# Optimization experiments

Measured on AMD Instinct MI355X. Metric: run time of the kernel, lower is better.

## Reference

```python
import jax, jax.numpy as jnp
import numpy as np
import math

PERIODS = [4, 2, 1]          # period_num[-3:] sorted desc
SEQ, PRED, CH = 192, 96, 8
TOPM, DM = 20, 512
N_TRAIN, BSZ = 10000, 32


def decompose_mg(data):
    # data: [N, L, C] -> mg: [P, N, L, C], offset-removed (last step per period)
    N, L, C = data.shape
    mgs = []
    for g in PERIODS:
        cur = data.reshape(N, L // g, g, C).mean(axis=2)   # pooled
        cur = jnp.repeat(cur, g, axis=1)                   # repeat_interleave
        mgs.append(cur)
    mg = jnp.stack(mgs, axis=0)                            # [P, N, L, C]
    offset = mg[:, :, -1:, :]
    return mg - offset


def l2norm(x, eps=1e-12):
    n = jnp.sqrt(jnp.sum(x * x, axis=-1, keepdims=True))
    return x / jnp.maximum(n, eps)


def setup_inputs() -> dict:
    key = jax.random.key(0)
    ks = jax.random.split(key, 10)
    F = SEQ * CH
    return {
        "x": jax.random.normal(ks[0], (BSZ, SEQ, CH), dtype=jnp.float32),
        "index": jax.random.randint(ks[1], (BSZ,), 0, N_TRAIN),
        "train_data_all": jax.random.normal(ks[2], (N_TRAIN, SEQ, CH), dtype=jnp.float32),
        "y_data_all": jax.random.normal(ks[3], (N_TRAIN, PRED, CH), dtype=jnp.float32),
        "W_sim": jax.random.normal(ks[4], (F, F), dtype=jnp.float32) / math.sqrt(F),
        "b_sim": jax.random.normal(ks[5], (F,), dtype=jnp.float32) * 0.01,
        "Wq": jax.random.normal(ks[6], (CH, DM), dtype=jnp.float32) / math.sqrt(CH),
        "bq": jax.random.normal(ks[7], (DM,), dtype=jnp.float32) * 0.01,
        "Wk": jax.random.normal(ks[8], (CH, DM), dtype=jnp.float32) / math.sqrt(CH),
        "bk": jax.random.normal(ks[9], (DM,), dtype=jnp.float32) * 0.01,
    }


def reference(x, index, train_data_all, y_data_all, W_sim, b_sim, Wq, bq, Wk, bk):
    P = len(PERIODS)
    bsz = x.shape[0]
    n_train = train_data_all.shape[0]

    # multi-period decomposition (prepare_dataset + retrieve)
    train_mg = decompose_mg(train_data_all)   # [P, N, SEQ, CH]
    y_mg = decompose_mg(y_data_all)           # [P, N, PRED, CH]
    x_mg = decompose_mg(x)                    # [P, B, SEQ, CH]

    # periodic_batch_corr: shared linear then cosine similarity
    bx = x_mg.reshape(P, bsz, -1) @ W_sim + b_sim           # [P, B, F]
    ax = train_mg.reshape(P, n_train, -1) @ W_sim + b_sim   # [P, N, F]
    sim = jnp.einsum('pbf,pnf->pbn', l2norm(bx), l2norm(ax))

    # self-exclusion sliding mask (train=True)
    win = 2 * (SEQ + PRED) - 1
    slid = jnp.arange(win)[None, :] + (index - SEQ - PRED + 1)[:, None]
    slid = jnp.clip(slid, 0, n_train - 1)
    mask = jnp.zeros((bsz, n_train), dtype=bool).at[
        jnp.arange(bsz)[:, None], slid].set(True)
    sim = jnp.where(mask[None], -jnp.inf, sim)

    # top-m retrieval
    _, topm_idx = jax.lax.top_k(sim, TOPM)                  # [P, B, TOPM]

    # gather neighbors per period
    gather = jax.vmap(lambda src, i: src[i])                # over period axis
    k = gather(train_mg, topm_idx)                          # [P, B, M, SEQ, CH]
    v = gather(y_mg, topm_idx)                              # [P, B, M, PRED, CH]

    # cross attention (shared projections across periods)
    q_emb = x_mg @ Wq + bq                                  # [P, B, S, D]
    k_emb = k @ Wk + bk                                     # [P, B, M, T, D]
    scores = jnp.einsum('pbsd,pbmtd->pbsmt', q_emb, k_emb) / math.sqrt(DM)
    S = scores.shape[2]
    w = jax.nn.softmax(scores.reshape(P, bsz, S, TOPM * S), axis=-1)
    w = w.reshape(P, bsz, S, TOPM, S)
    nw = w.sum(axis=-1).sum(axis=2)                         # [P, B, M]
    nw = jax.nn.softmax(nw, axis=-1)
    out = jnp.einsum('pbm,pbmlc->pblc', nw, v)              # [P, B, PRED, CH]
    return out
```

## Files before the change

### kernel.cpp

```cpp
#include <hip/hip_runtime.h>
#include <hip/hip_bf16.h>
#include <math.h>

#define NPER 3
#define SEQL 192
#define PREDL 96
#define CH 8
#define FD 1536
#define NT 10000
#define BS 32
#define PB 96
#define TOPM 20
#define DM 512
#define HALFW 287
#define NROWS 30000
#define NRP2 10112
#define NRB2 79
#define NCB 12
#define PCOLS 24
#define NWG2 (NRB2*NCB)
#define NJ 3840
#define K0R 384
#define K1R 768
#define K2R 1536
#define KS 16
#define NCH 4
#define CHSZ (NT/NCH)
#define NWTG 4080
#define NB_DOT (3*NRB2)
#define RSQRT_DM 0.04419417382415922f

typedef __attribute__((ext_vector_type(8))) short bf16x8;
typedef __attribute__((ext_vector_type(4))) float f32x4;
typedef __attribute__((address_space(3))) short lds_short_t;
typedef __attribute__((address_space(1))) const short glb_short_t;

__device__ inline float bflo(unsigned u){ return __uint_as_float(u << 16); }
__device__ inline float bfhi(unsigned u){ return __uint_as_float(u & 0xFFFF0000u); }
__device__ inline float bf2f(unsigned short u){ return __uint_as_float((unsigned)u << 16); }
__device__ inline unsigned short f2bf(float v){
  __hip_bfloat16 h = __float2bfloat16(v);
  return *reinterpret_cast<unsigned short*>(&h);
}

template<int L>
__device__ __forceinline__ void dec_body(const float* __restrict__ data,
                                         float* __restrict__ mg,
                                         __hip_bfloat16* __restrict__ m0,
                                         __hip_bfloat16* __restrict__ m1,
                                         __hip_bfloat16* __restrict__ m2,
                                         __hip_bfloat16* __restrict__ trH,
                                         __hip_bfloat16* __restrict__ trL,
                                         int N, int n, float* fpool) {
  float* row = fpool;
  float* m4  = fpool + L*CH;
  float* m2s = fpool + L*CH + (L/4)*CH;
  const float* src = data + (size_t)n*L*CH;
  for (int e = threadIdx.x; e < L*CH/4; e += 256)
    *reinterpret_cast<float4*>(&row[e*4]) = *reinterpret_cast<const float4*>(&src[e*4]);
  __syncthreads();
  for (int i = threadIdx.x; i < (L/4)*CH; i += 256) {
    int j = i >> 3, c = i & 7;
    m4[i] = (row[(4*j)*CH+c] + row[(4*j+1)*CH+c] + row[(4*j+2)*CH+c] + row[(4*j+3)*CH+c]) * 0.25f;
  }
  for (int i = threadIdx.x; i < (L/2)*CH; i += 256) {
    int j = i >> 3, c = i & 7;
    m2s[i] = (row[(2*j)*CH+c] + row[(2*j+1)*CH+c]) * 0.5f;
  }
  __syncthreads();
  if (mg) {
    size_t plane = (size_t)N*L*CH;
    size_t base  = (size_t)n*L*CH;
    for (int e = threadIdx.x; e < L*CH/4; e += 256) {
      int i = e*4;
      int l = i >> 3, c0 = i & 7;
      float v0[4], v1[4], v2[4];
      #pragma unroll
      for (int j=0;j<4;j++) {
        int c = c0 + j;
        v0[j] = m4[(l>>2)*CH+c] - m4[(L/4-1)*CH+c];
        v1[j] = m2s[(l>>1)*CH+c] - m2s[(L/2-1)*CH+c];
        v2[j] = row[i+j] - row[(L-1)*CH+c];
      }
      *reinterpret_cast<float4*>(&mg[base+i])           = make_float4(v0[0],v0[1],v0[2],v0[3]);
      *reinterpret_cast<float4*>(&mg[plane+base+i])     = make_float4(v1[0],v1[1],v1[2],v1[3]);
      *reinterpret_cast<float4*>(&mg[2*plane+base+i])   = make_float4(v2[0],v2[1],v2[2],v2[3]);
    }
  }
  if (m0) {
    unsigned short* p0 = (unsigned short*)m0 + (size_t)n*K0R;
    unsigned short* p1 = (unsigned short*)m1 + (size_t)n*K1R;
    unsigned short* p2 = (unsigned short*)m2 + (size_t)n*K2R;
    for (int e = threadIdx.x; e < K0R/4; e += 256) {
      int i = e*4, c0 = i & 7;
      ushort4 u;
      u.x = f2bf(m4[i]   - m4[(L/4-1)*CH + c0]);
      u.y = f2bf(m4[i+1] - m4[(L/4-1)*CH + c0+1]);
      u.z = f2bf(m4[i+2] - m4[(L/4-1)*CH + c0+2]);
      u.w = f2bf(m4[i+3] - m4[(L/4-1)*CH + c0+3]);
      *reinterpret_cast<ushort4*>(&p0[i]) = u;
    }
    for (int e = threadIdx.x; e < K1R/4; e += 256) {
      int i = e*4, c0 = i & 7;
      ushort4 u;
      u.x = f2bf(m2s[i]   - m2s[(L/2-1)*CH + c0]);
      u.y = f2bf(m2s[i+1] - m2s[(L/2-1)*CH + c0+1]);
      u.z = f2bf(m2s[i+2] - m2s[(L/2-1)*CH + c0+2]);
      u.w = f2bf(m2s[i+3] - m2s[(L/2-1)*CH + c0+3]);
      *reinterpret_cast<ushort4*>(&p1[i]) = u;
    }
    for (int e = threadIdx.x; e < K2R/4; e += 256) {
      int i = e*4, c0 = i & 7;
      ushort4 u;
      u.x = f2bf(row[i]   - row[(L-1)*CH + c0]);
      u.y = f2bf(row[i+1] - row[(L-1)*CH + c0+1]);
      u.z = f2bf(row[i+2] - row[(L-1)*CH + c0+2]);
      u.w = f2bf(row[i+3] - row[(L-1)*CH + c0+3]);
      *reinterpret_cast<ushort4*>(&p2[i]) = u;
    }
  }
  if (trH) {
    unsigned short* h = (unsigned short*)trH + (size_t)n*L*CH;
    unsigned short* l = (unsigned short*)trL + (size_t)n*L*CH;
    for (int e = threadIdx.x; e < L*CH/4; e += 256) {
      int i = e*4;
      ushort4 uh, ul;
      uh.x = f2bf(row[i]);   ul.x = f2bf(row[i]   - bf2f(uh.x));
      uh.y = f2bf(row[i+1]); ul.y = f2bf(row[i+1] - bf2f(uh.y));
      uh.z = f2bf(row[i+2]); ul.z = f2bf(row[i+2] - bf2f(uh.z));
      uh.w = f2bf(row[i+3]); ul.w = f2bf(row[i+3] - bf2f(uh.w));
      *reinterpret_cast<ushort4*>(&h[i]) = uh;
      *reinterpret_cast<ushort4*>(&l[i]) = ul;
    }
  }
}

__device__ __forceinline__ void wtg_body(const float* __restrict__ W,
                                         __hip_bfloat16* __restrict__ wt0,
                                         __hip_bfloat16* __restrict__ wt1,
                                         __hip_bfloat16* __restrict__ wt2,
                                         const float* __restrict__ Wq,
                                         const float* __restrict__ bq,
                                         const float* __restrict__ Wk,
                                         const float* __restrict__ bk,
                                         float* __restrict__ cst,
                                         int wb, float* fpool) {
  int bxx = wb / 48, byy = wb % 48;
  if (bxx == 84) {
    if (byy != 0) return;
    int tt = threadIdx.x;
    if (tt < 64) {
      int c = tt >> 3, e = tt & 7;
      float s = 0.f;
      for (int d=0; d<DM; d++) s += Wq[c*DM+d] * Wk[e*DM+d];
      cst[tt] = s;
    } else if (tt < 72) {
      int c = tt - 64; float s=0.f;
      for (int d=0;d<DM;d++) s += Wq[c*DM+d]*bk[d];
      cst[tt] = s;
    } else if (tt < 80) {
      int e = tt - 72; float s=0.f;
      for (int d=0;d<DM;d++) s += Wk[e*DM+d]*bq[d];
      cst[tt] = s;
    } else if (tt == 80) {
      float s=0.f;
      for (int d=0;d<DM;d++) s += bq[d]*bk[d];
      cst[80] = s;
    }
    return;
  }
  int G, kr0, Kred;
  __hip_bfloat16* Wt;
  if (bxx < 12)      { G = 4; kr0 = bxx*32;      Kred = K0R; Wt = wt0; }
  else if (bxx < 36) { G = 2; kr0 = (bxx-12)*32; Kred = K1R; Wt = wt1; }
  else               { G = 1; kr0 = (bxx-36)*32; Kred = K2R; Wt = wt2; }
  int f0 = byy*32;
  int k0 = kr0*G;
  int tid = threadIdx.x, tx = tid & 31, ty = tid >> 5;
  for (int i = ty; i < 32*G; i += 8)
    fpool[i*33 + tx] = W[(size_t)(k0+i)*FD + f0 + tx];
  __syncthreads();
  for (int fl = ty; fl < 32; fl += 8) {
    float s = 0.f;
    for (int i=0;i<G;i++) s += fpool[(((tx>>3)*G+i)*8 + (tx&7))*33 + fl];
    Wt[(size_t)(f0+fl)*Kred + kr0 + tx] = __float2bfloat16(s);
  }
}

__global__ __launch_bounds__(256) void k_front(const float* __restrict__ x,
                                               const float* __restrict__ train,
                                               float* __restrict__ x_mg,
                                               __hip_bfloat16* __restrict__ m0,
                                               __hip_bfloat16* __restrict__ m1,
                                               __hip_bfloat16* __restrict__ m2,
                                               __hip_bfloat16* __restrict__ trH,
                                               __hip_bfloat16* __restrict__ trL,
                                               const float* __restrict__ W,
                                               __hip_bfloat16* __restrict__ wt0,
                                               __hip_bfloat16* __restrict__ wt1,
                                               __hip_bfloat16* __restrict__ wt2,
                                               const float* __restrict__ Wq,
                                               const float* __restrict__ bq,
                                               const float* __restrict__ Wk,
                                               const float* __restrict__ bk,
                                               float* __restrict__ cst) {
  __shared__ float fpool[128*33];
  int bid = blockIdx.x;
  if (bid < NT) {
    dec_body<SEQL>(train, nullptr, m0, m1, m2, trH, trL, NT, bid, fpool);
  } else if (bid < NT + NWTG) {
    wtg_body(W, wt0, wt1, wt2, Wq, bq, Wk, bk, cst, bid - NT, fpool);
  } else {
    dec_body<SEQL>(x, x_mg, nullptr, nullptr, nullptr, nullptr, nullptr,
                   BS, bid - NT - NWTG, fpool);
  }
}

__global__ __launch_bounds__(256) void k_bx_part(const float* __restrict__ xmg,
                                                 const float* __restrict__ W,
                                                 float* __restrict__ bxp) {
  __shared__ float xs[PB][17];
  __shared__ float Ws[16][65];
  int f0 = blockIdx.x * 64;
  int ks = blockIdx.y;
  int kbase = ks * (FD/KS);
  int tid = threadIdx.x;
  int fl = tid & 63, gp = tid >> 6;
  float acc[24];
  #pragma unroll
  for (int j=0;j<24;j++) acc[j]=0.f;
  for (int k0 = kbase; k0 < kbase + FD/KS; k0 += 16) {
    for (int e = tid; e < PB*16; e += 256) {
      int r = e >> 4, k = e & 15;
      xs[r][k] = xmg[(size_t)r*FD + k0 + k];
    }
    for (int e = tid; e < 16*64; e += 256) {
      int k = e >> 6, f = e & 63;
      Ws[k][f] = W[(size_t)(k0+k)*FD + f0 + f];
    }
    __syncthreads();
    #pragma unroll
    for (int kk = 0; kk < 16; kk++) {
      float w = Ws[kk][fl];
      #pragma unroll
      for (int j=0;j<24;j++) acc[j] += w * xs[gp + 4*j][kk];
    }
    __syncthreads();
  }
  #pragma unroll
  for (int j=0;j<24;j++) {
    int pb = gp + 4*j;
    bxp[((size_t)ks*PB + pb)*FD + f0 + fl] = acc[j];
  }
}

__global__ __launch_bounds__(256) void k_bxnorm(const float* __restrict__ bxp,
                                                const float* __restrict__ bsim,
                                                float* __restrict__ u_out,
                                                float* __restrict__ cpb) {
  __shared__ float rowv[FD];
  __shared__ float r1[256], r2[256];
  __shared__ float invs;
  int pb = blockIdx.x, tid = threadIdx.x;
  float s2 = 0.f, sb = 0.f;
  for (int f = tid; f < FD; f += 256) {
    float s = 0.f;
    #pragma unroll
    for (int ks=0; ks<KS; ks++) s += bxp[((size_t)ks*PB + pb)*FD + f];
    s += bsim[f];
    rowv[f] = s;
    s2 += s*s; sb += s*bsim[f];
  }
  r1[tid]=s2; r2[tid]=sb; __syncthreads();
  for (int off=128; off>0; off>>=1) {
    if (tid<off) { r1[tid]+=r1[tid+off]; r2[tid]+=r2[tid+off]; }
    __syncthreads();
  }
  if (tid==0) {
    float iv = 1.f / fmaxf(sqrtf(r1[0]), 1e-12f);
    invs = iv;
    cpb[pb] = r2[0] * iv;
  }
  __syncthreads();
  float iv = invs;
  for (int f = tid; f < FD; f += 256) u_out[(size_t)pb*FD + f] = rowv[f]*iv;
}

__global__ __launch_bounds__(256) void k_t_part(const float* __restrict__ u,
                                                const float* __restrict__ W,
                                                float* __restrict__ tp) {
  __shared__ float us[PB][17];
  __shared__ float Wt[64][17];
  int k0 = blockIdx.x * 64;
  int ks = blockIdx.y;
  int fbase = ks * (FD/KS);
  int tid = threadIdx.x;
  int kl = tid & 63, gp = tid >> 6;
  float acc[24];
  #pragma unroll
  for (int j=0;j<24;j++) acc[j]=0.f;
  for (int fc = fbase; fc < fbase + FD/KS; fc += 16) {
    for (int e = tid; e < PB*16; e += 256) {
      int r = e >> 4, f = e & 15;
      us[r][f] = u[(size_t)r*FD + fc + f];
    }
    for (int e = tid; e < 64*16; e += 256) {
      int k = e >> 4, f = e & 15;
      Wt[k][f] = W[(size_t)(k0+k)*FD + fc + f];
    }
    __syncthreads();
    #pragma unroll
    for (int ff = 0; ff < 16; ff++) {
      float w = Wt[kl][ff];
      #pragma unroll
      for (int j=0;j<24;j++) acc[j] += w * us[gp + 4*j][ff];
    }
    __syncthreads();
  }
  #pragma unroll
  for (int j=0;j<24;j++) {
    int pb = gp + 4*j;
    tp[((size_t)ks*PB + pb)*FD + k0 + kl] = acc[j];
  }
}

__global__ __launch_bounds__(192) void k_tred_adj(const float* __restrict__ tp,
                                                  __hip_bfloat16* __restrict__ tadjH,
                                                  __hip_bfloat16* __restrict__ tadjL) {
  __shared__ float ts[SEQL*CH];
  __shared__ float Tc[CH];
  int pb = blockIdx.x;
  int p = pb / BS;
  int g = (p==0) ? 4 : (p==1) ? 2 : 1;
  int l = threadIdx.x;
  #pragma unroll
  for (int c=0;c<CH;c++) {
    float s = 0.f;
    #pragma unroll
    for (int ks=0; ks<KS; ks++) s += tp[((size_t)ks*PB + pb)*FD + l*CH + c];
    ts[l*CH+c] = s;
  }
  __syncthreads();
  if (l < CH) {
    float s=0.f;
    for (int j=0;j<SEQL;j++) s += ts[j*CH+l];
    Tc[l] = s;
  }
  __syncthreads();
  int j0 = (l/g)*g;
  bool last = (j0 == SEQL-g);
  float ig = 1.f/(float)g;
  unsigned short* th = (unsigned short*)tadjH;
  unsigned short* tl = (unsigned short*)tadjL;
  #pragma unroll
  for (int c=0;c<CH;c++) {
    float s = 0.f;
    for (int jj=0;jj<g;jj++) s += ts[(j0+jj)*CH+c];
    float v = s*ig - (last ? Tc[c]*ig : 0.f);
    unsigned short hv = f2bf(v);
    th[(size_t)pb*FD + l*CH+c] = hv;
    tl[(size_t)pb*FD + l*CH+c] = f2bf(v - bf2f(hv));
  }
}

__device__ __forceinline__ void norm_body(const short* __restrict__ A,
                                          const short* __restrict__ B,
                                          int K, int p, int seg,
                                          const float* __restrict__ bsim,
                                          float* __restrict__ part,
                                          short* pool) {
  short* lA = pool;
  short* lB = pool + 128*32;
  int q = NWG2 >> 3, r = NWG2 & 7;
  int xcd = seg & 7, pos = seg >> 3;
  int wgid = (xcd < r ? xcd*(q+1) : r*(q+1) + (xcd-r)*q) + pos;
  int rb = wgid / NCB, cb = wgid - rb*NCB;
  int row0 = rb*128, col0 = cb*128;
  int tid = threadIdx.x, lane = tid & 63, wid = tid >> 6;
  int wr = (wid>>1)*64, wc = (wid&1)*64;

  size_t aoff[2], boff[2];
  int ldsb[2];
  #pragma unroll
  for (int i=0;i<2;i++) {
    int lrow = (wid*2+i)*16 + (lane>>2);
    int sl = lane & 3;
    int ss = (sl - lrow - (lrow>>2)) & 3;
    aoff[i] = (size_t)(row0 + lrow)*K + 8*ss;
    boff[i] = (size_t)(col0 + lrow)*K + 8*ss;
    ldsb[i] = (wid*2+i)*16*32;
  }

  f32x4 acc[4][4];
  #pragma unroll
  for (int m=0;m<4;m++)
    #pragma unroll
    for (int n=0;n<4;n++) acc[m][n] = (f32x4){0.f,0.f,0.f,0.f};

  int kslot = lane >> 4;
  for (int k0 = 0; k0 < K; k0 += 32) {
    #pragma unroll
    for (int i=0;i<2;i++) {
      __builtin_amdgcn_global_load_lds((glb_short_t*)(A + aoff[i] + k0),
                                       (lds_short_t*)&lA[ldsb[i]], 16, 0, 0);
      __builtin_amdgcn_global_load_lds((glb_short_t*)(B + boff[i] + k0),
                                       (lds_short_t*)&lB[ldsb[i]], 16, 0, 0);
    }
    __syncthreads();
    bf16x8 af[4], bfr[4];
    #pragma unroll
    for (int m=0;m<4;m++) {
      int rr = wr + m*16 + (lane&15);
      int s = (kslot + rr + (rr>>2)) & 3;
      af[m] = *(const bf16x8*)&lA[rr*32 + s*8];
    }
    #pragma unroll
    for (int n=0;n<4;n++) {
      int rr = wc + n*16 + (lane&15);
      int s = (kslot + rr + (rr>>2)) & 3;
      bfr[n] = *(const bf16x8*)&lB[rr*32 + s*8];
    }
    #pragma unroll
    for (int m=0;m<4;m++)
      #pragma unroll
      for (int n=0;n<4;n++)
        acc[m][n] = __builtin_amdgcn_mfma_f32_16x16x32_bf16(af[m], bfr[n], acc[m][n], 0, 0, 0);
    __syncthreads();
  }

  float bv[4];
  #pragma unroll
  for (int n=0;n<4;n++) bv[n] = bsim[col0 + wc + n*16 + (lane&15)];
  int pslot = cb*2 + (wid&1);
  #pragma unroll
  for (int m=0;m<4;m++) {
    #pragma unroll
    for (int j=0;j<4;j++) {
      float s = 0.f;
      #pragma unroll
      for (int n=0;n<4;n++) { float v = acc[m][n][j] + bv[n]; s += v*v; }
      s += __shfl_xor(s, 1); s += __shfl_xor(s, 2);
      s += __shfl_xor(s, 4); s += __shfl_xor(s, 8);
      if ((lane & 15) == 0) {
        int rr = row0 + wr + m*16 + (lane>>4)*4 + j;
        part[((size_t)p*NRP2 + rr)*PCOLS + pslot] = s;
      }
    }
  }
}

__device__ __forceinline__ void dot_body(const short* __restrict__ A,
                                         const short* __restrict__ B,
                                         float* __restrict__ dst,
                                         int cbn, short* pool) {
  short* lA = pool;
  short* lB = pool + 128*32;
  int col0 = cbn * 128;
  int tid = threadIdx.x, lane = tid & 63, wid = tid >> 6;
  int wr = (wid>>1)*64, wc = (wid&1)*64;

  size_t aoff[2], boff[2];
  int ldsb[2];
  #pragma unroll
  for (int i=0;i<2;i++) {
    int lrow = (wid*2+i)*16 + (lane>>2);
    int sl = lane & 3;
    int ss = (sl - lrow - (lrow>>2)) & 3;
    aoff[i] = (size_t)lrow*FD + 8*ss;
    boff[i] = (size_t)(col0 + lrow)*FD + 8*ss;
    ldsb[i] = (wid*2+i)*16*32;
  }

  f32x4 acc[4][4];
  #pragma unroll
  for (int m=0;m<4;m++)
    #pragma unroll
    for (int n=0;n<4;n++) acc[m][n] = (f32x4){0.f,0.f,0.f,0.f};

  int kslot = lane >> 4;
  for (int k0 = 0; k0 < FD; k0 += 32) {
    #pragma unroll
    for (int i=0;i<2;i++) {
      __builtin_amdgcn_global_load_lds((glb_short_t*)(A + aoff[i] + k0),
                                       (lds_short_t*)&lA[ldsb[i]], 16, 0, 0);
      __builtin_amdgcn_global_load_lds((glb_short_t*)(B + boff[i] + k0),
                                       (lds_short_t*)&lB[ldsb[i]], 16, 0, 0);
    }
    __syncthreads();
    bf16x8 af[4], bfr[4];
    #pragma unroll
    for (int m=0;m<4;m++) {
      int rr = wr + m*16 + (lane&15);
      int s = (kslot + rr + (rr>>2)) & 3;
      af[m] = *(const bf16x8*)&lA[rr*32 + s*8];
    }
    #pragma unroll
    for (int n=0;n<4;n++) {
      int rr = wc + n*16 + (lane&15);
      int s = (kslot + rr + (rr>>2)) & 3;
      bfr[n] = *(const bf16x8*)&lB[rr*32 + s*8];
    }
    #pragma unroll
    for (int m=0;m<4;m++)
      #pragma unroll
      for (int n=0;n<4;n++)
        acc[m][n] = __builtin_amdgcn_mfma_f32_16x16x32_bf16(af[m], bfr[n], acc[m][n], 0, 0, 0);
    __syncthreads();
  }

  #pragma unroll
  for (int m=0;m<4;m++) {
    int prow = wr + m*16 + (lane>>4)*4;
    if (prow >= PB) continue;
    #pragma unroll
    for (int n=0;n<4;n++) {
      int ncol = col0 + wc + n*16 + (lane&15);
      if (ncol >= NT) continue;
      #pragma unroll
      for (int j=0;j<4;j++) {
        dst[(size_t)(prow + j)*NT + ncol] = acc[m][n][j];
      }
    }
  }
}

__global__ __launch_bounds__(256) void k_gemms(
    const __hip_bfloat16* __restrict__ A0b, const __hip_bfloat16* __restrict__ A1b,
    const __hip_bfloat16* __restrict__ A2b,
    const __hip_bfloat16* __restrict__ B0b, const __hip_bfloat16* __restrict__ B1b,
    const __hip_bfloat16* __restrict__ B2b,
    const float* __restrict__ bsim, float* __restrict__ part,
    const __hip_bfloat16* __restrict__ tadjHb, const __hip_bfloat16* __restrict__ tadjLb,
    const __hip_bfloat16* __restrict__ trHb, const __hip_bfloat16* __restrict__ trLb,
    float* __restrict__ dotp3) {
  __shared__ __align__(16) short pool[2*128*32];
  int bid = blockIdx.x;
  if (bid < NB_DOT) {
    int term = bid / NRB2, cbn = bid - term*NRB2;
    const short* A = (term == 2) ? (const short*)tadjLb : (const short*)tadjHb;
    const short* B = (term == 1) ? (const short*)trLb   : (const short*)trHb;
    dot_body(A, B, dotp3 + (size_t)term*PB*NT, cbn, pool);
  } else if (bid < NB_DOT + NWG2) {
    norm_body((const short*)A2b, (const short*)B2b, K2R, 2, bid - NB_DOT, bsim, part, pool);
  } else if (bid < NB_DOT + 2*NWG2) {
    norm_body((const short*)A1b, (const short*)B1b, K1R, 1, bid - NB_DOT - NWG2, bsim, part, pool);
  } else {
    norm_body((const short*)A0b, (const short*)B0b, K0R, 0,
              bid - NB_DOT - 2*NWG2, bsim, part, pool);
  }
}

__global__ __launch_bounds__(256) void k_topk_part(const float* __restrict__ dotp3,
                                                   const float* __restrict__ cpb,
                                                   const float* __restrict__ part,
                                                   const int* __restrict__ index,
                                                   float* __restrict__ cv,
                                                   int* __restrict__ ci) {
  __shared__ float vals[CHSZ];
  __shared__ float rv[4];
  __shared__ int   ri[4];
  int pb = blockIdx.x, ch = blockIdx.y;
  int p = pb / BS, b = pb - p*BS;
  int n0 = ch*CHSZ;
  int tid = threadIdx.x, lane = tid & 63, wv = tid >> 6;
  int idx = index[b];
  int bl = idx - HALFW; if (bl < 0) bl = 0;
  int bh = idx + HALFW; if (bh > NT-1) bh = NT-1;
  float cp = cpb[pb];
  for (int i = tid; i < CHSZ; i += 256) {
    int n = n0 + i;
    const float* pr = &part[((size_t)p*NRP2 + n)*PCOLS];
    float s2 = 0.f;
    #pragma unroll
    for (int cb2=0; cb2<PCOLS; cb2++) s2 += pr[cb2];
    float d = dotp3[(size_t)pb*NT + n]
            + dotp3[(size_t)PB*NT + (size_t)pb*NT + n]
            + dotp3[2*(size_t)PB*NT + (size_t)pb*NT + n] + cp;
    float v = d / fmaxf(sqrtf(s2), 1e-12f);
    if (n >= bl && n <= bh) v = -INFINITY;
    vals[i] = v;
  }
  __syncthreads();
  for (int it = 0; it < TOPM; it++) {
    float bv = -INFINITY; int bi = CHSZ;
    for (int i = tid; i < CHSZ; i += 256) {
      float v = vals[i];
      if (v > bv) { bv = v; bi = i; }
    }
    #pragma unroll
    for (int off=32; off>0; off>>=1) {
      float ov = __shfl_xor(bv, off);
      int   oi = __shfl_xor(bi, off);
      if (ov > bv || (ov == bv && oi < bi)) { bv = ov; bi = oi; }
    }
    if (lane == 0) { rv[wv] = bv; ri[wv] = bi; }
    __syncthreads();
    if (tid == 0) {
      float fv = rv[0]; int fi = ri[0];
      #pragma unroll
      for (int w2=1; w2<4; w2++)
        if (rv[w2] > fv || (rv[w2] == fv && ri[w2] < fi)) { fv = rv[w2]; fi = ri[w2]; }
      cv[(pb*NCH + ch)*TOPM + it] = fv;
      ci[(pb*NCH + ch)*TOPM + it] = n0 + fi;
      vals[fi] = -INFINITY;
    }
    __syncthreads();
  }
}

__global__ __launch_bounds__(64) void k_topk_merge(const float* __restrict__ cv,
                                                   const int* __restrict__ ci,
                                                   int* __restrict__ topm) {
  __shared__ float v[NCH*TOPM];
  __shared__ int   id[NCH*TOPM];
  int pb = blockIdx.x;
  int lane = threadIdx.x;
  for (int i = lane; i < NCH*TOPM; i += 64) {
    v[i]  = cv[pb*NCH*TOPM + i];
    id[i] = ci[pb*NCH*TOPM + i];
  }
  __syncthreads();
  for (int it = 0; it < TOPM; it++) {
    float bv = -INFINITY; int bi = 0x7fffffff;
    for (int i = lane; i < NCH*TOPM; i += 64) {
      float vv = v[i];
      int ii = id[i];
      if (vv > bv || (vv == bv && ii < bi)) { bv = vv; bi = ii; }
    }
    #pragma unroll
    for (int off=32; off>0; off>>=1) {
      float ov = __shfl_xor(bv, off);
      int   oi = __shfl_xor(bi, off);
      if (ov > bv || (ov == bv && oi < bi)) { bv = ov; bi = oi; }
    }
    if (lane == 0) topm[pb*TOPM + it] = bi;
    for (int i = lane; i < NCH*TOPM; i += 64)
      if (id[i] == bi) v[i] = -INFINITY;
    __syncthreads();
  }
}

__device__ __forceinline__ void v_body(const float* __restrict__ ydata,
                                       const int* __restrict__ topm,
                                       float* __restrict__ vbuf,
                                       int bm, float* bpool) {
  float* row = bpool;
  float* m4  = bpool + 768;
  float* m2  = bpool + 960;
  int pb = bm / TOPM;
  int p = pb / BS;
  int n = topm[bm];
  int tid = threadIdx.x;
  const float* src = ydata + (size_t)n*PREDL*CH;
  for (int i=tid; i<PREDL*CH; i+=256) row[i]=src[i];
  __syncthreads();
  for (int i=tid; i<(PREDL/4)*CH; i+=256) {
    int j=i>>3, c=i&7;
    m4[i] = (row[(4*j)*CH+c]+row[(4*j+1)*CH+c]+row[(4*j+2)*CH+c]+row[(4*j+3)*CH+c])*0.25f;
  }
  for (int i=tid; i<(PREDL/2)*CH; i+=256) {
    int j=i>>3, c=i&7;
    m2[i] = (row[(2*j)*CH+c]+row[(2*j+1)*CH+c])*0.5f;
  }
  __syncthreads();
  float* dst = vbuf + (size_t)bm*PREDL*CH;
  for (int i=tid; i<PREDL*CH; i+=256) {
    int l=i>>3, c=i&7;
    float v;
    if (p==0)      v = m4[(l>>2)*CH+c] - m4[(PREDL/4-1)*CH+c];
    else if (p==1) v = m2[(l>>1)*CH+c] - m2[(PREDL/2-1)*CH+c];
    else           v = row[i] - row[(PREDL-1)*CH+c];
    dst[i] = v;
  }
}

template<int SH>
__device__ __forceinline__ void scores_body(
    const short* __restrict__ plane, int Kp,
    int pb, int sg,
    const int* __restrict__ topm,
    const float* __restrict__ xmg,
    const float* __restrict__ cst,
    float* __restrict__ nws,
    float* sc, int* tl, float* wred, float* lcst) {
  constexpr int UNQ = SEQL >> SH;
  constexpr int J   = TOPM * UNQ;
  constexpr int NU  = (J + 255) >> 8;
  constexpr bool FULL = (J % 256 == 0);
  int tid = threadIdx.x;
  int lane = tid & 63, wv = tid >> 6;
  if (tid < TOPM) tl[tid] = topm[pb*TOPM + tid];
  if (tid >= 32 && tid < 32+81) lcst[tid-32] = cst[tid-32];
  __syncthreads();
  uint4 kreg[NU];
  #pragma unroll
  for (int u=0; u<NU; u++) {
    int j = tid + u*256;
    if (FULL || j < J) {
      int m = j / UNQ, jj = j - m*UNQ;
      kreg[u] = *reinterpret_cast<const uint4*>(plane + (size_t)tl[m]*Kp + jj*8);
    }
  }
  for (int s8 = 0; s8 < 8; s8++) {
    int s = sg*8 + s8;
    int qr = pb*SEQL + s;
    float4 qa = *reinterpret_cast<const float4*>(&xmg[(size_t)qr*8]);
    float4 qc = *reinterpret_cast<const float4*>(&xmg[(size_t)qr*8+4]);
    float xq[8] = {qa.x,qa.y,qa.z,qa.w,qc.x,qc.y,qc.z,qc.w};
    float q[8];
    #pragma unroll
    for (int e=0;e<8;e++) {
      float ss = lcst[72+e];
      #pragma unroll
      for (int c=0;c<8;c++) ss += xq[c]*lcst[c*8+e];
      q[e] = ss;
    }
    float qb_s = lcst[80];
    #pragma unroll
    for (int c=0;c<8;c++) qb_s += xq[c]*lcst[64+c];
    float ms[NU];
    float lmax = -INFINITY;
    #pragma unroll
    for (int u=0; u<NU; u++) {
      int j = tid + u*256;
      if (FULL || j < J) {
        uint4 w = kreg[u];
        float s0 = qb_s;
        s0 += q[0]*bflo(w.x) + q[1]*bfhi(w.x);
        s0 += q[2]*bflo(w.y) + q[3]*bfhi(w.y);
        s0 += q[4]*bflo(w.z) + q[5]*bfhi(w.z);
        s0 += q[6]*bflo(w.w) + q[7]*bfhi(w.w);
        s0 *= RSQRT_DM;
        ms[u] = s0;
        lmax = fmaxf(lmax, s0);
      } else ms[u] = -INFINITY;
    }
    #pragma unroll
    for (int off=32; off>0; off>>=1) lmax = fmaxf(lmax, __shfl_xor(lmax, off));
    if (lane==0) wred[wv] = lmax;
    __syncthreads();
    float mx = fmaxf(fmaxf(wred[0],wred[1]),fmaxf(wred[2],wred[3]));
    float lsum = 0.f;
    #pragma unroll
    for (int u=0; u<NU; u++) {
      int j = tid + u*256;
      if (FULL || j < J) {
        float e = __expf(ms[u]-mx);
        sc[j] = e;
        lsum += e;
      }
    }
    #pragma unroll
    for (int off=32; off>0; off>>=1) lsum += __shfl_xor(lsum, off);
    if (lane==0) wred[4+wv] = lsum;
    __syncthreads();
    float invZ = 1.f / (wred[4]+wred[5]+wred[6]+wred[7]);
    for (int m = wv; m < TOPM; m += 4) {
      float v = 0.f;
      #pragma unroll
      for (int jj = 0; jj < UNQ; jj += 64) {
        int j2 = jj + lane;
        if (UNQ % 64 == 0 || j2 < UNQ) v += sc[m*UNQ + j2];
      }
      #pragma unroll
      for (int off=32; off>0; off>>=1) v += __shfl_xor(v, off);
      if (lane==0) nws[((size_t)pb*SEQL + s)*TOPM + m] = v * invZ;
    }
    __syncthreads();
  }
}

__global__ __launch_bounds__(256) void k_back(const __hip_bfloat16* __restrict__ m0,
                                              const __hip_bfloat16* __restrict__ m1,
                                              const __hip_bfloat16* __restrict__ m2,
                                              const int* __restrict__ topm,
                                              const float* __restrict__ xmg,
                                              const float* __restrict__ cst,
                                              float* __restrict__ nws,
                                              const float* __restrict__ ydata,
                                              float* __restrict__ vbuf) {
  __shared__ float bpool[3968];
  int bid = blockIdx.x;
  if (bid < PB*24) {
    int pb = bid / 24, sg = bid - (bid/24)*24;
    int p = pb / BS;
    float* sc = bpool;
    int* tl = (int*)(bpool + 3840);
    float* wred = bpool + 3864;
    float* lcst = bpool + 3872;
    if (p == 0)
      scores_body<2>((const short*)m0, K0R, pb, sg, topm, xmg, cst, nws, sc, tl, wred, lcst);
    else if (p == 1)
      scores_body<1>((const short*)m1, K1R, pb, sg, topm, xmg, cst, nws, sc, tl, wred, lcst);
    else
      scores_body<0>((const short*)m2, K2R, pb, sg, topm, xmg, cst, nws, sc, tl, wred, lcst);
  } else {
    v_body(ydata, topm, vbuf, bid - PB*24, bpool);
  }
}

__global__ __launch_bounds__(256) void k_out(const float* __restrict__ nws,
                                             const float* __restrict__ vbuf,
                                             float* __restrict__ out) {
  __shared__ float nwp[TOPM];
  __shared__ float nwf[TOPM];
  int pb = blockIdx.x;
  int tid = threadIdx.x;
  if (tid < TOPM) {
    float s=0.f;
    for (int ss=0; ss<SEQL; ss++) s += nws[((size_t)pb*SEQL+ss)*TOPM + tid];
    nwp[tid] = s;
  }
  __syncthreads();
  if (tid==0) {
    float mx=-INFINITY;
    for (int m=0;m<TOPM;m++) mx=fmaxf(mx,nwp[m]);
    float Z=0.f;
    for (int m=0;m<TOPM;m++){ float e=expf(nwp[m]-mx); nwf[m]=e; Z+=e; }
    float iz=1.f/Z;
    for (int m=0;m<TOPM;m++) nwf[m]*=iz;
  }
  __syncthreads();
  for (int i=tid; i<PREDL*CH; i+=256) {
    float o=0.f;
    #pragma unroll
    for (int m=0;m<TOPM;m++) o += nwf[m]*vbuf[((size_t)pb*TOPM+m)*PREDL*CH + i];
    out[(size_t)pb*PREDL*CH + i] = o;
  }
}

extern "C" void kernel_launch(void* const* d_in, const int* in_sizes, int n_in,
                              void* d_out, int out_size, void* d_ws, size_t ws_size,
                              hipStream_t stream) {
  const float* x     = (const float*)d_in[0];
  const int*   index = (const int*)  d_in[1];
  const float* train = (const float*)d_in[2];
  const float* ydata = (const float*)d_in[3];
  const float* Wsim  = (const float*)d_in[4];
  const float* bsim  = (const float*)d_in[5];
  const float* Wq    = (const float*)d_in[6];
  const float* bq    = (const float*)d_in[7];
  const float* Wk    = (const float*)d_in[8];
  const float* bk    = (const float*)d_in[9];
  float* out = (float*)d_out;

  float* ws = (float*)d_ws;
  size_t off = 0;
  auto alloc = [&](size_t n)->float* { float* pp = ws + off; off += (n + 63) & ~(size_t)63; return pp; };
  __hip_bfloat16* m0b = (__hip_bfloat16*)alloc((size_t)NRP2*K0R/2);
  __hip_bfloat16* m1b = (__hip_bfloat16*)alloc((size_t)NRP2*K1R/2);
  __hip_bfloat16* m2b = (__hip_bfloat16*)alloc((size_t)NRP2*K2R/2);
  __hip_bfloat16* wt0 = (__hip_bfloat16*)alloc((size_t)FD*K0R/2);
  __hip_bfloat16* wt1 = (__hip_bfloat16*)alloc((size_t)FD*K1R/2);
  __hip_bfloat16* wt2 = (__hip_bfloat16*)alloc((size_t)FD*K2R/2);
  __hip_bfloat16* trH = (__hip_bfloat16*)alloc((size_t)NRP2*FD/2);
  __hip_bfloat16* trL = (__hip_bfloat16*)alloc((size_t)NRP2*FD/2);
  __hip_bfloat16* tadjH = (__hip_bfloat16*)alloc((size_t)128*FD/2);
  __hip_bfloat16* tadjL = (__hip_bfloat16*)alloc((size_t)128*FD/2);
  float* x_mg     = alloc((size_t)NPER*BS*FD);
  float* bx       = alloc((size_t)PB*FD);
  float* cpb      = alloc(PB);
  float* gpart    = alloc((size_t)KS*PB*FD);
  float* part     = alloc((size_t)NPER*NRP2*PCOLS);
  float* dotp3    = alloc((size_t)3*PB*NT);
  float* cv       = alloc((size_t)PB*NCH*TOPM);
  int*   ci       = (int*)alloc(PB*NCH*TOPM);
  int*   topm     = (int*)alloc(PB*TOPM);
  float* cst      = alloc(128);
  float* vbuf     = alloc((size_t)PB*TOPM*PREDL*CH);
  float* nws      = alloc((size_t)PB*SEQL*TOPM);
  if (off * sizeof(float) > ws_size) return;

  k_front<<<NT + NWTG + BS, 256, 0, stream>>>(x, train, x_mg, m0b, m1b, m2b, trH, trL,
                                              Wsim, wt0, wt1, wt2, Wq, bq, Wk, bk, cst);
  k_bx_part<<<dim3(24, KS), 256, 0, stream>>>(x_mg, Wsim, gpart);
  k_bxnorm<<<PB, 256, 0, stream>>>(gpart, bsim, bx, cpb);
  k_t_part<<<dim3(24, KS), 256, 0, stream>>>(bx, Wsim, gpart);
  k_tred_adj<<<PB, 192, 0, stream>>>(gpart, tadjH, tadjL);
  k_gemms<<<NB_DOT + 3*NWG2, 256, 0, stream>>>(m0b, m1b, m2b, wt0, wt1, wt2, bsim, part,
                                               tadjH, tadjL, trH, trL, dotp3);
  k_topk_part<<<dim3(PB, NCH), 256, 0, stream>>>(dotp3, cpb, part, index, cv, ci);
  k_topk_merge<<<PB, 64, 0, stream>>>(cv, ci, topm);
  k_back<<<PB*24 + PB*TOPM, 256, 0, stream>>>(m0b, m1b, m2b, topm, x_mg, cst, nws,
                                              ydata, vbuf);
  k_out<<<PB, 256, 0, stream>>>(nws, vbuf, out);
}
```

Measured before the change: 432.3 us.

## Double-buffer LDS tiles in GEMM bodies to overlap global loads with MFMA

Result: faster. 412.8 us (-4.5%).

```diff
diff --git a/kernel.cpp b/kernel.cpp
--- a/kernel.cpp
+++ b/kernel.cpp
@@ -28,6 +28,7 @@
 #define CHSZ (NT/NCH)
 #define NWTG 4080
 #define NB_DOT (3*NRB2)
+#define BUFSZ (2*128*32)
 #define RSQRT_DM 0.04419417382415922f
 
 typedef __attribute__((ext_vector_type(8))) short bf16x8;
@@ -369,8 +370,6 @@
                                           const float* __restrict__ bsim,
                                           float* __restrict__ part,
                                           short* pool) {
-  short* lA = pool;
-  short* lB = pool + 128*32;
   int q = NWG2 >> 3, r = NWG2 & 7;
   int xcd = seg & 7, pos = seg >> 3;
   int wgid = (xcd < r ? xcd*(q+1) : r*(q+1) + (xcd-r)*q) + pos;
@@ -398,15 +397,28 @@
     for (int n=0;n<4;n++) acc[m][n] = (f32x4){0.f,0.f,0.f,0.f};
 
   int kslot = lane >> 4;
+  #pragma unroll
+  for (int i=0;i<2;i++) {
+    __builtin_amdgcn_global_load_lds((glb_short_t*)(A + aoff[i]),
+                                     (lds_short_t*)&pool[ldsb[i]], 16, 0, 0);
+    __builtin_amdgcn_global_load_lds((glb_short_t*)(B + boff[i]),
+                                     (lds_short_t*)&pool[128*32 + ldsb[i]], 16, 0, 0);
+  }
+  __syncthreads();
+  int cur = 0;
   for (int k0 = 0; k0 < K; k0 += 32) {
-    #pragma unroll
-    for (int i=0;i<2;i++) {
-      __builtin_amdgcn_global_load_lds((glb_short_t*)(A + aoff[i] + k0),
-                                       (lds_short_t*)&lA[ldsb[i]], 16, 0, 0);
-      __builtin_amdgcn_global_load_lds((glb_short_t*)(B + boff[i] + k0),
-                                       (lds_short_t*)&lB[ldsb[i]], 16, 0, 0);
-    }
-    __syncthreads();
+    if (k0 + 32 < K) {
+      short* nb = pool + (cur^1)*BUFSZ;
+      #pragma unroll
+      for (int i=0;i<2;i++) {
+        __builtin_amdgcn_global_load_lds((glb_short_t*)(A + aoff[i] + k0 + 32),
+                                         (lds_short_t*)&nb[ldsb[i]], 16, 0, 0);
+        __builtin_amdgcn_global_load_lds((glb_short_t*)(B + boff[i] + k0 + 32),
+                                         (lds_short_t*)&nb[128*32 + ldsb[i]], 16, 0, 0);
+      }
+    }
+    const short* lA = pool + cur*BUFSZ;
+    const short* lB = pool + cur*BUFSZ + 128*32;
     bf16x8 af[4], bfr[4];
     #pragma unroll
     for (int m=0;m<4;m++) {
@@ -426,6 +438,7 @@
       for (int n=0;n<4;n++)
         acc[m][n] = __builtin_amdgcn_mfma_f32_16x16x32_bf16(af[m], bfr[n], acc[m][n], 0, 0, 0);
     __syncthreads();
+    cur ^= 1;
   }
 
   float bv[4];
@@ -453,8 +466,6 @@
                                          const short* __restrict__ B,
                                          float* __restrict__ dst,
                                          int cbn, short* pool) {
-  short* lA = pool;
-  short* lB = pool + 128*32;
   int col0 = cbn * 128;
   int tid = threadIdx.x, lane = tid & 63, wid = tid >> 6;
   int wr = (wid>>1)*64, wc = (wid&1)*64;
@@ -478,15 +489,28 @@
     for (int n=0;n<4;n++) acc[m][n] = (f32x4){0.f,0.f,0.f,0.f};
 
   int kslot = lane >> 4;
+  #pragma unroll
+  for (int i=0;i<2;i++) {
+    __builtin_amdgcn_global_load_lds((glb_short_t*)(A + aoff[i]),
+                                     (lds_short_t*)&pool[ldsb[i]], 16, 0, 0);
+    __builtin_amdgcn_global_load_lds((glb_short_t*)(B + boff[i]),
+                                     (lds_short_t*)&pool[128*32 + ldsb[i]], 16, 0, 0);
+  }
+  __syncthreads();
+  int cur = 0;
   for (int k0 = 0; k0 < FD; k0 += 32) {
-    #pragma unroll
-    for (int i=0;i<2;i++) {
-      __builtin_amdgcn_global_load_lds((glb_short_t*)(A + aoff[i] + k0),
-                                       (lds_short_t*)&lA[ldsb[i]], 16, 0, 0);
-      __builtin_amdgcn_global_load_lds((glb_short_t*)(B + boff[i] + k0),
-                                       (lds_short_t*)&lB[ldsb[i]], 16, 0, 0);
-    }
-    __syncthreads();
+    if (k0 + 32 < FD) {
+      short* nb = pool + (cur^1)*BUFSZ;
+      #pragma unroll
+      for (int i=0;i<2;i++) {
+        __builtin_amdgcn_global_load_lds((glb_short_t*)(A + aoff[i] + k0 + 32),
+                                         (lds_short_t*)&nb[ldsb[i]], 16, 0, 0);
+        __builtin_amdgcn_global_load_lds((glb_short_t*)(B + boff[i] + k0 + 32),
+                                         (lds_short_t*)&nb[128*32 + ldsb[i]], 16, 0, 0);
+      }
+    }
+    const short* lA = pool + cur*BUFSZ;
+    const short* lB = pool + cur*BUFSZ + 128*32;
     bf16x8 af[4], bfr[4];
     #pragma unroll
     for (int m=0;m<4;m++) {
@@ -506,6 +530,7 @@
       for (int n=0;n<4;n++)
         acc[m][n] = __builtin_amdgcn_mfma_f32_16x16x32_bf16(af[m], bfr[n], acc[m][n], 0, 0, 0);
     __syncthreads();
+    cur ^= 1;
   }
 
   #pragma unroll
@@ -533,7 +558,7 @@
     const __hip_bfloat16* __restrict__ tadjHb, const __hip_bfloat16* __restrict__ tadjLb,
     const __hip_bfloat16* __restrict__ trHb, const __hip_bfloat16* __restrict__ trLb,
     float* __restrict__ dotp3) {
-  __shared__ __align__(16) short pool[2*128*32];
+  __shared__ __align__(16) short pool[2*BUFSZ];
   int bid = blockIdx.x;
   if (bid < NB_DOT) {
     int term = bid / NRB2, cbn = bid - term*NRB2;
```
